# Performance work log

Measured on AMD Instinct MI355X. Metric: run time of the kernel, lower is better.

Reference implementation:

```python
import jax, jax.numpy as jnp
import numpy as np

B, C, H, W = 2, 256, 192, 192
STRIDE = 8


def conv2d(x, w, b, pad_h, pad_w):
    y = jax.lax.conv_general_dilated(
        x, w, window_strides=(1, 1),
        padding=[(pad_h, pad_h), (pad_w, pad_w)],
        dimension_numbers=('NCHW', 'OIHW', 'NCHW'))
    return y + b[None, :, None, None]


def rotated_feature_align(feat, boxes, spatial_scale):
    # feat: [B,C,Hf,Wf]; boxes: [B,Hf*Wf,5] per-pixel rboxes in image coords.
    # points=1: bilinearly sample feat at each pixel's box center and add to feat,
    # matching mmcv's rotated_feature_align forward kernel (incl. its (y,x) read order
    # and ROI-Align-style border handling).
    Bf, Cf, Hf, Wf = feat.shape
    y = boxes[..., 0].reshape(Bf, Hf, Wf) * spatial_scale
    x = boxes[..., 1].reshape(Bf, Hf, Wf) * spatial_scale
    valid = (y >= -1.0) & (y <= Hf) & (x >= -1.0) & (x <= Wf)
    y = jnp.maximum(y, 0.0)
    x = jnp.maximum(x, 0.0)
    yl0 = jnp.floor(y).astype(jnp.int32)
    xl0 = jnp.floor(x).astype(jnp.int32)
    ey = yl0 >= Hf - 1
    ex = xl0 >= Wf - 1
    yl = jnp.where(ey, Hf - 1, yl0)
    yh = jnp.where(ey, Hf - 1, jnp.minimum(yl0 + 1, Hf - 1))
    xl = jnp.where(ex, Wf - 1, xl0)
    xh = jnp.where(ex, Wf - 1, jnp.minimum(xl0 + 1, Wf - 1))
    y = jnp.where(ey, jnp.asarray(Hf - 1, feat.dtype), y)
    x = jnp.where(ex, jnp.asarray(Wf - 1, feat.dtype), x)
    ly = y - yl.astype(feat.dtype)
    lx = x - xl.astype(feat.dtype)
    hy = 1.0 - ly
    hx = 1.0 - lx
    ft = jnp.transpose(feat, (0, 2, 3, 1))  # [B,Hf,Wf,C]
    bi = jnp.arange(Bf)[:, None, None]
    v = ((hy * hx)[..., None] * ft[bi, yl, xl]
         + (hy * lx)[..., None] * ft[bi, yl, xh]
         + (ly * hx)[..., None] * ft[bi, yh, xl]
         + (ly * lx)[..., None] * ft[bi, yh, xh])
    v = jnp.where(valid[..., None], v, 0.0)
    return feat + jnp.transpose(v, (0, 3, 1, 2))


def setup_inputs() -> dict:
    key = jax.random.key(0)
    ks = jax.random.split(key, 9)
    x = jax.random.normal(ks[0], (B, C, H, W), dtype=jnp.float32)
    img = float(H * STRIDE)
    cy = jax.random.uniform(ks[1], (B, H * W), minval=0.0, maxval=img)
    cx = jax.random.uniform(ks[2], (B, H * W), minval=0.0, maxval=img)
    bw = jax.random.uniform(ks[3], (B, H * W), minval=8.0, maxval=64.0)
    bh = jax.random.uniform(ks[4], (B, H * W), minval=8.0, maxval=64.0)
    ba = jax.random.uniform(ks[5], (B, H * W), minval=-np.pi / 2, maxval=np.pi / 2)
    best_rbboxes = jnp.stack([cy, cx, bw, bh, ba], axis=-1)  # [B, H*W, 5]
    std = 0.01  # normal_init(std=0.01)
    w51 = jax.random.normal(ks[6], (C, C, 5, 1), dtype=jnp.float32) * std
    w15 = jax.random.normal(ks[7], (C, C, 1, 5), dtype=jnp.float32) * std
    w11 = jax.random.normal(ks[8], (C, C, 1, 1), dtype=jnp.float32) * std
    b51 = jnp.zeros((C,), jnp.float32)
    b15 = jnp.zeros((C,), jnp.float32)
    b11 = jnp.zeros((C,), jnp.float32)
    return {"x": x, "best_rbboxes": best_rbboxes, "w51": w51, "b51": b51,
            "w15": w15, "b15": b15, "w11": w11, "b11": b11}


def reference(x, best_rbboxes, w51, b51, w15, b15, w11, b11):
    # conv_5_1(conv_1_5(x)) + conv_1_1(x), then rotated feature alignment, then residual.
    feat = conv2d(conv2d(x, w15, b15, 0, 2), w51, b51, 2, 0) + conv2d(x, w11, b11, 0, 0)
    refined = rotated_feature_align(feat, best_rbboxes, 1.0 / STRIDE)
    return x + refined
```

## Files before the change

kernel.cpp:

```cpp
#include <hip/hip_runtime.h>
#include <hip/hip_bf16.h>
#include <stdint.h>

#define B_ 2
#define C_ 256
#define H_ 192
#define W_ 192
#define HW_ (H_*W_)
#define CHW_ (C_*HW_)
#define P_ (B_*HW_)
#define SCALE 0.125f

typedef __attribute__((ext_vector_type(8))) short bf16x8;
typedef __attribute__((ext_vector_type(4))) float f32x4;

__device__ __forceinline__ void gload_lds16(const void* g, void* l) {
  __builtin_amdgcn_global_load_lds(
      (const __attribute__((address_space(1))) uint32_t*)g,
      (__attribute__((address_space(3))) uint32_t*)l, 16, 0, 0);
}

__global__ __launch_bounds__(256) void wtrans_kernel(
    const float* __restrict__ w15, const float* __restrict__ w51,
    const float* __restrict__ w11,
    __hip_bfloat16* __restrict__ w1t, __hip_bfloat16* __restrict__ w2t,
    __hip_bfloat16* __restrict__ zbuf) {
  int i = blockIdx.x * 256 + threadIdx.x;
  if (i < C_ * C_ * 5) {
    int co = i / (C_ * 5);
    int r  = i - co * (C_ * 5);
    int ci = r / 5;
    int k  = r - ci * 5;
    w1t[(size_t)co * 1280 + k * 256 + ci] = __float2bfloat16(w15[i]);
    w2t[(size_t)co * 1536 + k * 256 + ci] = __float2bfloat16(w51[i]);
  }
  if (i < C_ * C_) {
    int co = i >> 8, ci = i & 255;
    w2t[(size_t)co * 1536 + 1280 + ci] = __float2bfloat16(w11[i]);
  }
  if (i < 1024) zbuf[i] = __float2bfloat16(0.f);
}

__global__ __launch_bounds__(256) void nchw2nhwc_kernel(
    const float* __restrict__ x, __hip_bfloat16* __restrict__ xT) {
  __shared__ float tile[64][65];
  const int p0 = blockIdx.x * 64, c0 = blockIdx.y * 64, b = blockIdx.z;
  const int tid = threadIdx.x;
  const float* xb = x + (size_t)b * CHW_;
  {
    const int cr = tid >> 4;
    const int pc = (tid & 15) * 4;
#pragma unroll
    for (int j = 0; j < 4; ++j) {
      float4 v = *(const float4*)(xb + (size_t)(c0 + cr + j * 16) * HW_ + p0 + pc);
      *(float4*)&tile[cr + j * 16][pc] = v;
    }
  }
  __syncthreads();
  {
    const int pr = tid >> 2;
    const int cc = (tid & 3) * 16;
    union { unsigned short u[16]; uint4 q[2]; } wpk;
#pragma unroll
    for (int j = 0; j < 16; ++j) {
      __hip_bfloat16 hb = __float2bfloat16(tile[cc + j][pr]);
      wpk.u[j] = *(unsigned short*)&hb;
    }
    char* xo = (char*)(xT + ((size_t)b * HW_ + p0 + pr) * C_ + c0 + cc);
    *(uint4*)xo = wpk.q[0];
    *(uint4*)(xo + 16) = wpk.q[1];
  }
}

#define AB1 25600
__global__ __launch_bounds__(256, 3) void gemm1_kernel(
    const __hip_bfloat16* __restrict__ xT, const __hip_bfloat16* __restrict__ w1t,
    const float* __restrict__ b15, __hip_bfloat16* __restrict__ t1,
    const __hip_bfloat16* __restrict__ zbuf) {
  __shared__ __align__(16) char lds[AB1 + 16384];
  int bid = blockIdx.x;
  bid = (bid & 7) * 96 + (bid >> 3);
  const int nb = bid & 1, bh = bid >> 1;
  const int p0 = bh * 192;
  const int tid = threadIdx.x, l = tid & 63, wid = tid >> 6;
  const int wrow = (wid >> 1) * 96, wcol = (wid & 1) * 64;
  const int sboff = (((l & 7) ^ (l >> 3)) << 4);
  const int lrow = l >> 3;
  const int corow0 = nb * 128;

  int b_ad[4][2];
#pragma unroll
  for (int n = 0; n < 4; ++n)
#pragma unroll
    for (int kk = 0; kk < 2; ++kk)
      b_ad[n][kk] = AB1 + (wcol + n * 16 + (l & 15)) * 128 +
                    (((kk * 4 + (l >> 4)) ^ ((l & 15) & 7)) << 4);

  f32x4 acc[6][4] = {};
  const char* xTb = (const char*)xT;
  const char* wB  = (const char*)w1t;
  const char* zb  = (const char*)zbuf;

  for (int cib = 0; cib < 4; ++cib) {
    for (int is = wid; is < 25; is += 4) {
      int row = is * 8 + lrow;
      const char* src = ((unsigned)(row - 4) < 192u)
          ? xTb + (size_t)(p0 + row - 4) * 512 + cib * 128 + sboff
          : zb + sboff;
      gload_lds16(src, lds + is * 1024);
    }
    for (int k = 0; k < 5; ++k) {
      int boff = k * 512 + cib * 128;
#pragma unroll
      for (int ii = 0; ii < 4; ++ii) {
        int is = wid * 4 + ii;
        const char* bs = wB + (size_t)(corow0 + is * 8 + lrow) * 2560 + boff + sboff;
        gload_lds16(bs, lds + AB1 + is * 1024);
      }
      __syncthreads();
      int x8 = ((l & 15) + k + 2) & 7;
      int arow0 = wrow + (l & 15) + k + 2;
#pragma unroll
      for (int kk = 0; kk < 2; ++kk) {
        int ablk = ((kk * 4 + (l >> 4)) ^ x8) << 4;
        bf16x8 bfr[4];
#pragma unroll
        for (int n = 0; n < 4; ++n) bfr[n] = *(const bf16x8*)(lds + b_ad[n][kk]);
#pragma unroll
        for (int m = 0; m < 6; ++m) {
          bf16x8 af = *(const bf16x8*)(lds + (arow0 + m * 16) * 128 + ablk);
#pragma unroll
          for (int n = 0; n < 4; ++n)
            acc[m][n] = __builtin_amdgcn_mfma_f32_16x16x32_bf16(af, bfr[n], acc[m][n], 0, 0, 0);
        }
      }
      __syncthreads();
    }
  }
#pragma unroll
  for (int n = 0; n < 4; ++n) {
    int co = corow0 + wcol + n * 16 + (l & 15);
    float bias = b15[co];
#pragma unroll
    for (int m = 0; m < 6; ++m) {
      int prow = p0 + wrow + m * 16 + (l >> 4) * 4;
#pragma unroll
      for (int r = 0; r < 4; ++r)
        t1[(size_t)(prow + r) * 256 + co] = __float2bfloat16(acc[m][n][r] + bias);
    }
  }
}

#define AB2 24576
__global__ __launch_bounds__(256, 3) void gemm2_kernel(
    const __hip_bfloat16* __restrict__ t1, const __hip_bfloat16* __restrict__ xT,
    const __hip_bfloat16* __restrict__ w2t,
    const float* __restrict__ b51, const float* __restrict__ b11,
    __hip_bfloat16* __restrict__ featT, const __hip_bfloat16* __restrict__ zbuf) {
  __shared__ __align__(16) char lds[AB2 + 16384];
  int bid = blockIdx.x;
  bid = (bid & 7) * 96 + (bid >> 3);
  const int nb = bid & 1, bh = bid >> 1;
  const int p0 = bh * 192;
  const int h = bh % 192;
  const int tid = threadIdx.x, l = tid & 63, wid = tid >> 6;
  const int wrow = (wid >> 1) * 96, wcol = (wid & 1) * 64;
  const int sboff = (((l & 7) ^ (l >> 3)) << 4);
  const int lrow = l >> 3;
  const int corow0 = nb * 128;

  int a_ad[6][2], b_ad[4][2];
#pragma unroll
  for (int m = 0; m < 6; ++m)
#pragma unroll
    for (int kk = 0; kk < 2; ++kk)
      a_ad[m][kk] = (wrow + m * 16 + (l & 15)) * 128 +
                    (((kk * 4 + (l >> 4)) ^ ((l & 15) & 7)) << 4);
#pragma unroll
  for (int n = 0; n < 4; ++n)
#pragma unroll
    for (int kk = 0; kk < 2; ++kk)
      b_ad[n][kk] = AB2 + (wcol + n * 16 + (l & 15)) * 128 +
                    (((kk * 4 + (l >> 4)) ^ ((l & 15) & 7)) << 4);

  f32x4 acc[6][4] = {};
  const char* t1b = (const char*)t1;
  const char* xTb = (const char*)xT;
  const char* wB  = (const char*)w2t;
  const char* zb  = (const char*)zbuf;

  for (int s = 0; s < 24; ++s) {
    const char* abase;
    int boff;
    if (s < 20) {
      int k = s >> 2, cib = s & 3, dl = k - 2;
      abase = ((unsigned)(h + dl) < 192u)
          ? t1b + (size_t)(p0 + dl * 192) * 512 + cib * 128
          : (const char*)0;
      boff = k * 512 + cib * 128;
    } else {
      abase = xTb + (size_t)p0 * 512 + (s - 20) * 128;
      boff = 2560 + (s - 20) * 128;
    }
    for (int is = wid; is < 24; is += 4) {
      int row = is * 8 + lrow;
      const char* src = abase ? abase + (size_t)row * 512 + sboff : zb + sboff;
      gload_lds16(src, lds + is * 1024);
    }
#pragma unroll
    for (int ii = 0; ii < 4; ++ii) {
      int is = wid * 4 + ii;
      const char* bs = wB + (size_t)(corow0 + is * 8 + lrow) * 3072 + boff + sboff;
      gload_lds16(bs, lds + AB2 + is * 1024);
    }
    __syncthreads();
#pragma unroll
    for (int kk = 0; kk < 2; ++kk) {
      bf16x8 bfr[4];
#pragma unroll
      for (int n = 0; n < 4; ++n) bfr[n] = *(const bf16x8*)(lds + b_ad[n][kk]);
#pragma unroll
      for (int m = 0; m < 6; ++m) {
        bf16x8 af = *(const bf16x8*)(lds + a_ad[m][kk]);
#pragma unroll
        for (int n = 0; n < 4; ++n)
          acc[m][n] = __builtin_amdgcn_mfma_f32_16x16x32_bf16(af, bfr[n], acc[m][n], 0, 0, 0);
      }
    }
    __syncthreads();
  }
#pragma unroll
  for (int n = 0; n < 4; ++n) {
    int co = corow0 + wcol + n * 16 + (l & 15);
    float bias = b51[co] + b11[co];
#pragma unroll
    for (int m = 0; m < 6; ++m) {
      int prow = p0 + wrow + m * 16 + (l >> 4) * 4;
#pragma unroll
      for (int r = 0; r < 4; ++r)
        featT[(size_t)(prow + r) * 256 + co] = __float2bfloat16(acc[m][n][r] + bias);
    }
  }
}

__global__ __launch_bounds__(256) void align_kernel(
    const __hip_bfloat16* __restrict__ xT, const __hip_bfloat16* __restrict__ featT,
    const float* __restrict__ boxes, float* __restrict__ out) {
  __shared__ float vs[16][258];
  const int tid = threadIdx.x, l = tid & 63, wv = tid >> 6;
  const int p0 = blockIdx.x * 16;

#pragma unroll
  for (int i = 0; i < 2; ++i) {
    int pl = wv * 4 + i * 2 + (l >> 5);
    int p = p0 + pl;
    int b = p / HW_;
    int p2 = p - b * HW_;
    float yy = boxes[(size_t)p * 5 + 0] * SCALE;
    float xx = boxes[(size_t)p * 5 + 1] * SCALE;
    bool valid = (yy >= -1.0f) && (yy <= (float)H_) && (xx >= -1.0f) && (xx <= (float)W_);
    yy = fmaxf(yy, 0.f);
    xx = fmaxf(xx, 0.f);
    int yl = (int)floorf(yy), xl = (int)floorf(xx);
    int yh, xh;
    if (yl >= H_ - 1) { yl = H_ - 1; yh = H_ - 1; yy = (float)(H_ - 1); } else { yh = yl + 1; }
    if (xl >= W_ - 1) { xl = W_ - 1; xh = W_ - 1; xx = (float)(W_ - 1); } else { xh = xl + 1; }
    float ly = yy - (float)yl, lx = xx - (float)xl;
    float hy = 1.f - ly, hx = 1.f - lx;
    float q00 = hy * hx, q01 = hy * lx, q10 = ly * hx, q11 = ly * lx;
    if (!valid) { q00 = 0.f; q01 = 0.f; q10 = 0.f; q11 = 0.f; }
    const unsigned short* fT = (const unsigned short*)featT + (size_t)b * HW_ * C_;
    const unsigned short* xb = (const unsigned short*)xT + (size_t)b * HW_ * C_;
    int co = (l & 31) * 8;
    uint4 A  = *(const uint4*)(fT + ((size_t)yl * W_ + xl) * C_ + co);
    uint4 Bv = *(const uint4*)(fT + ((size_t)yl * W_ + xh) * C_ + co);
    uint4 Cv = *(const uint4*)(fT + ((size_t)yh * W_ + xl) * C_ + co);
    uint4 D  = *(const uint4*)(fT + ((size_t)yh * W_ + xh) * C_ + co);
    uint4 E  = *(const uint4*)(fT + (size_t)p2 * C_ + co);
    uint4 X  = *(const uint4*)(xb + (size_t)p2 * C_ + co);
    float o[8];
#pragma unroll
    for (int w = 0; w < 4; ++w) {
      unsigned int aw = (&A.x)[w], bw = (&Bv.x)[w], cw = (&Cv.x)[w],
                   dw = (&D.x)[w], ew = (&E.x)[w], xw = (&X.x)[w];
      float a0 = __uint_as_float(aw << 16), a1 = __uint_as_float(aw & 0xffff0000u);
      float b0 = __uint_as_float(bw << 16), b1 = __uint_as_float(bw & 0xffff0000u);
      float c0 = __uint_as_float(cw << 16), c1 = __uint_as_float(cw & 0xffff0000u);
      float d0 = __uint_as_float(dw << 16), d1 = __uint_as_float(dw & 0xffff0000u);
      float e0 = __uint_as_float(ew << 16), e1 = __uint_as_float(ew & 0xffff0000u);
      float x0 = __uint_as_float(xw << 16), x1 = __uint_as_float(xw & 0xffff0000u);
      o[w * 2 + 0] = x0 + e0 + q00 * a0 + q01 * b0 + q10 * c0 + q11 * d0;
      o[w * 2 + 1] = x1 + e1 + q00 * a1 + q01 * b1 + q10 * c1 + q11 * d1;
    }
    *(float4*)&vs[pl][co]     = make_float4(o[0], o[1], o[2], o[3]);
    *(float4*)&vs[pl][co + 4] = make_float4(o[4], o[5], o[6], o[7]);
  }
  __syncthreads();

  const int pl = tid & 15, cg = tid >> 4;
  const int p = p0 + pl;
  const int b = p / HW_;
  const int p2 = p - b * HW_;
  float* oc = out + (size_t)b * CHW_ + p2;
#pragma unroll
  for (int j = 0; j < 16; ++j) {
    int ch = cg * 16 + j;
    __builtin_nontemporal_store(vs[pl][ch], &oc[(size_t)ch * HW_]);
  }
}

extern "C" void kernel_launch(void* const* d_in, const int* in_sizes, int n_in,
                              void* d_out, int out_size, void* d_ws, size_t ws_size,
                              hipStream_t stream) {
  const float* x     = (const float*)d_in[0];
  const float* boxes = (const float*)d_in[1];
  const float* w51   = (const float*)d_in[2];
  const float* b51   = (const float*)d_in[3];
  const float* w15   = (const float*)d_in[4];
  const float* b15   = (const float*)d_in[5];
  const float* w11   = (const float*)d_in[6];
  const float* b11   = (const float*)d_in[7];
  float* out = (float*)d_out;

  __hip_bfloat16* featT = (__hip_bfloat16*)d_ws;
  __hip_bfloat16* xT   = featT + (size_t)P_ * C_;
  __hip_bfloat16* w1t  = xT + (size_t)P_ * C_;
  __hip_bfloat16* w2t  = w1t + (size_t)C_ * 1280;
  __hip_bfloat16* zbuf = w2t + (size_t)C_ * 1536;
  __hip_bfloat16* t1 = (__hip_bfloat16*)d_out;

  wtrans_kernel<<<dim3((C_ * C_ * 5 + 255) / 256), 256, 0, stream>>>(
      w15, w51, w11, w1t, w2t, zbuf);
  nchw2nhwc_kernel<<<dim3(HW_ / 64, C_ / 64, B_), 256, 0, stream>>>(x, xT);
  gemm1_kernel<<<dim3(768), 256, 0, stream>>>(xT, w1t, b15, t1, zbuf);
  gemm2_kernel<<<dim3(768), 256, 0, stream>>>(t1, xT, w2t, b51, b11, featT, zbuf);
  align_kernel<<<dim3(P_ / 16), 256, 0, stream>>>(xT, featT, boxes, out);
}
```

Before: 172.5 us.

## Double-buffer gemm2 with 512-thread 384-row tiles and interleaved prefetch

Rewrites the second conv GEMM so each 512-thread block computes a 384-row by 128-channel tile, covering two image rows, with double-buffered LDS for A and B. The next K-step's global-to-LDS loads are issued in chunks between MFMA phases, replacing the old load-sync-compute-sync loop. Wave priority is raised around MFMA bursts and explicit waitcnts and barriers order the stages. The aim is to hide global load latency behind MFMA work. In exchange, the 128KB LDS allocation allows only one block per CU, and 384 blocks give an uneven final wave.

New measurement: 191.7 us. 11.1% more time.

```diff
diff --git a/kernel.cpp b/kernel.cpp
--- a/kernel.cpp
+++ b/kernel.cpp
@@ -151,83 +151,145 @@
   }
 }
 
-#define AB2 24576
-__global__ __launch_bounds__(256, 3) void gemm2_kernel(
+#define G2_AB 49152
+#define G2_BB 98304
+__global__ __launch_bounds__(512, 2) void gemm2_kernel(
     const __hip_bfloat16* __restrict__ t1, const __hip_bfloat16* __restrict__ xT,
     const __hip_bfloat16* __restrict__ w2t,
     const float* __restrict__ b51, const float* __restrict__ b11,
     __hip_bfloat16* __restrict__ featT, const __hip_bfloat16* __restrict__ zbuf) {
-  __shared__ __align__(16) char lds[AB2 + 16384];
+  __shared__ __align__(16) char lds[131072];
   int bid = blockIdx.x;
-  bid = (bid & 7) * 96 + (bid >> 3);
+  bid = (bid & 7) * 48 + (bid >> 3);
   const int nb = bid & 1, bh = bid >> 1;
-  const int p0 = bh * 192;
-  const int h = bh % 192;
+  const int p0 = bh * 384;
+  const int hv0 = (2 * bh) % 192;
   const int tid = threadIdx.x, l = tid & 63, wid = tid >> 6;
   const int wrow = (wid >> 1) * 96, wcol = (wid & 1) * 64;
   const int sboff = (((l & 7) ^ (l >> 3)) << 4);
   const int lrow = l >> 3;
   const int corow0 = nb * 128;
 
-  int a_ad[6][2], b_ad[4][2];
-#pragma unroll
-  for (int m = 0; m < 6; ++m)
-#pragma unroll
-    for (int kk = 0; kk < 2; ++kk)
-      a_ad[m][kk] = (wrow + m * 16 + (l & 15)) * 128 +
-                    (((kk * 4 + (l >> 4)) ^ ((l & 15) & 7)) << 4);
-#pragma unroll
-  for (int n = 0; n < 4; ++n)
-#pragma unroll
-    for (int kk = 0; kk < 2; ++kk)
-      b_ad[n][kk] = AB2 + (wcol + n * 16 + (l & 15)) * 128 +
-                    (((kk * 4 + (l >> 4)) ^ ((l & 15) & 7)) << 4);
-
-  f32x4 acc[6][4] = {};
   const char* t1b = (const char*)t1;
   const char* xTb = (const char*)xT;
   const char* wB  = (const char*)w2t;
   const char* zb  = (const char*)zbuf;
 
-  for (int s = 0; s < 24; ++s) {
-    const char* abase;
-    int boff;
+  auto stA = [&](int s, int buf, int i0, int i1) {
+    const char* base;
+    bool v0, v1;
     if (s < 20) {
       int k = s >> 2, cib = s & 3, dl = k - 2;
-      abase = ((unsigned)(h + dl) < 192u)
-          ? t1b + (size_t)(p0 + dl * 192) * 512 + cib * 128
-          : (const char*)0;
-      boff = k * 512 + cib * 128;
+      base = t1b + (ptrdiff_t)(p0 + dl * 192) * 512 + cib * 128;
+      v0 = (unsigned)(hv0 + dl) < 192u;
+      v1 = (unsigned)(hv0 + 1 + dl) < 192u;
     } else {
-      abase = xTb + (size_t)p0 * 512 + (s - 20) * 128;
-      boff = 2560 + (s - 20) * 128;
-    }
-    for (int is = wid; is < 24; is += 4) {
-      int row = is * 8 + lrow;
-      const char* src = abase ? abase + (size_t)row * 512 + sboff : zb + sboff;
-      gload_lds16(src, lds + is * 1024);
-    }
-#pragma unroll
-    for (int ii = 0; ii < 4; ++ii) {
-      int is = wid * 4 + ii;
-      const char* bs = wB + (size_t)(corow0 + is * 8 + lrow) * 3072 + boff + sboff;
-      gload_lds16(bs, lds + AB2 + is * 1024);
-    }
-    __syncthreads();
-#pragma unroll
-    for (int kk = 0; kk < 2; ++kk) {
-      bf16x8 bfr[4];
-#pragma unroll
-      for (int n = 0; n < 4; ++n) bfr[n] = *(const bf16x8*)(lds + b_ad[n][kk]);
-#pragma unroll
-      for (int m = 0; m < 6; ++m) {
-        bf16x8 af = *(const bf16x8*)(lds + a_ad[m][kk]);
-#pragma unroll
-        for (int n = 0; n < 4; ++n)
-          acc[m][n] = __builtin_amdgcn_mfma_f32_16x16x32_bf16(af, bfr[n], acc[m][n], 0, 0, 0);
-      }
-    }
-    __syncthreads();
+      base = xTb + (size_t)p0 * 512 + (s - 20) * 128;
+      v0 = v1 = true;
+    }
+#pragma unroll
+    for (int i = i0; i < i1; ++i) {
+      int slot = i * 8 + wid;
+      int row = slot * 8 + lrow;
+      bool ok = (row < 192) ? v0 : v1;
+      const char* src = ok ? base + (size_t)row * 512 + sboff : zb + sboff;
+      gload_lds16(src, lds + buf * G2_AB + slot * 1024);
+    }
+  };
+  auto stB = [&](int s, int buf) {
+    int boff = (s < 20) ? (s >> 2) * 512 + (s & 3) * 128 : 2560 + (s - 20) * 128;
+#pragma unroll
+    for (int i = 0; i < 2; ++i) {
+      int slot = i * 8 + wid;
+      const char* bs = wB + (size_t)(corow0 + slot * 8 + lrow) * 3072 + boff + sboff;
+      gload_lds16(bs, lds + G2_BB + buf * 16384 + slot * 1024);
+    }
+  };
+
+  int a_ad[6][2], b_ad[4][2];
+#pragma unroll
+  for (int m = 0; m < 6; ++m)
+#pragma unroll
+    for (int kk = 0; kk < 2; ++kk)
+      a_ad[m][kk] = (wrow + m * 16 + (l & 15)) * 128 +
+                    (((kk * 4 + (l >> 4)) ^ ((l & 15) & 7)) << 4);
+#pragma unroll
+  for (int n = 0; n < 4; ++n)
+#pragma unroll
+    for (int kk = 0; kk < 2; ++kk)
+      b_ad[n][kk] = (wcol + n * 16 + (l & 15)) * 128 +
+                    (((kk * 4 + (l >> 4)) ^ ((l & 15) & 7)) << 4);
+
+  f32x4 acc[6][4] = {};
+  stA(0, 0, 0, 6);
+  stB(0, 0);
+  asm volatile("s_waitcnt vmcnt(0)" ::: "memory");
+  __builtin_amdgcn_s_barrier();
+
+  for (int t = 0; t < 24; ++t) {
+    const int cur = t & 1, nxt = cur ^ 1;
+    const char* la = lds + cur * G2_AB;
+    const char* lb = lds + G2_BB + cur * 16384;
+    if (t > 0) asm volatile("s_waitcnt vmcnt(0)" ::: "memory");
+    bf16x8 af[6], bfr[2];
+#pragma unroll
+    for (int m = 0; m < 6; ++m) af[m] = *(const bf16x8*)(la + a_ad[m][0]);
+    bfr[0] = *(const bf16x8*)(lb + b_ad[0][0]);
+    bfr[1] = *(const bf16x8*)(lb + b_ad[1][0]);
+    if (t < 23) stA(t + 1, nxt, 0, 4);
+    __builtin_amdgcn_s_barrier();
+    asm volatile("s_waitcnt lgkmcnt(0)" ::: "memory");
+    __builtin_amdgcn_sched_barrier(0);
+    __builtin_amdgcn_s_setprio(1);
+#pragma unroll
+    for (int m = 0; m < 6; ++m) {
+      acc[m][0] = __builtin_amdgcn_mfma_f32_16x16x32_bf16(af[m], bfr[0], acc[m][0], 0, 0, 0);
+      acc[m][1] = __builtin_amdgcn_mfma_f32_16x16x32_bf16(af[m], bfr[1], acc[m][1], 0, 0, 0);
+    }
+    __builtin_amdgcn_s_setprio(0);
+    __builtin_amdgcn_s_barrier();
+    bfr[0] = *(const bf16x8*)(lb + b_ad[2][0]);
+    bfr[1] = *(const bf16x8*)(lb + b_ad[3][0]);
+    if (t < 23) { stA(t + 1, nxt, 4, 6); stB(t + 1, nxt); }
+    __builtin_amdgcn_s_barrier();
+    asm volatile("s_waitcnt lgkmcnt(0)" ::: "memory");
+    __builtin_amdgcn_sched_barrier(0);
+    __builtin_amdgcn_s_setprio(1);
+#pragma unroll
+    for (int m = 0; m < 6; ++m) {
+      acc[m][2] = __builtin_amdgcn_mfma_f32_16x16x32_bf16(af[m], bfr[0], acc[m][2], 0, 0, 0);
+      acc[m][3] = __builtin_amdgcn_mfma_f32_16x16x32_bf16(af[m], bfr[1], acc[m][3], 0, 0, 0);
+    }
+    __builtin_amdgcn_s_setprio(0);
+    __builtin_amdgcn_s_barrier();
+#pragma unroll
+    for (int m = 0; m < 6; ++m) af[m] = *(const bf16x8*)(la + a_ad[m][1]);
+    bfr[0] = *(const bf16x8*)(lb + b_ad[0][1]);
+    bfr[1] = *(const bf16x8*)(lb + b_ad[1][1]);
+    __builtin_amdgcn_s_barrier();
+    asm volatile("s_waitcnt lgkmcnt(0)" ::: "memory");
+    __builtin_amdgcn_sched_barrier(0);
+    __builtin_amdgcn_s_setprio(1);
+#pragma unroll
+    for (int m = 0; m < 6; ++m) {
+      acc[m][0] = __builtin_amdgcn_mfma_f32_16x16x32_bf16(af[m], bfr[0], acc[m][0], 0, 0, 0);
+      acc[m][1] = __builtin_amdgcn_mfma_f32_16x16x32_bf16(af[m], bfr[1], acc[m][1], 0, 0, 0);
+    }
+    __builtin_amdgcn_s_setprio(0);
+    __builtin_amdgcn_s_barrier();
+    bfr[0] = *(const bf16x8*)(lb + b_ad[2][1]);
+    bfr[1] = *(const bf16x8*)(lb + b_ad[3][1]);
+    __builtin_amdgcn_s_barrier();
+    asm volatile("s_waitcnt lgkmcnt(0)" ::: "memory");
+    __builtin_amdgcn_sched_barrier(0);
+    __builtin_amdgcn_s_setprio(1);
+#pragma unroll
+    for (int m = 0; m < 6; ++m) {
+      acc[m][2] = __builtin_amdgcn_mfma_f32_16x16x32_bf16(af[m], bfr[0], acc[m][2], 0, 0, 0);
+      acc[m][3] = __builtin_amdgcn_mfma_f32_16x16x32_bf16(af[m], bfr[1], acc[m][3], 0, 0, 0);
+    }
+    __builtin_amdgcn_s_setprio(0);
+    __builtin_amdgcn_s_barrier();
   }
 #pragma unroll
   for (int n = 0; n < 4; ++n) {
@@ -333,6 +395,6 @@
       w15, w51, w11, w1t, w2t, zbuf);
   nchw2nhwc_kernel<<<dim3(HW_ / 64, C_ / 64, B_), 256, 0, stream>>>(x, xT);
   gemm1_kernel<<<dim3(768), 256, 0, stream>>>(xT, w1t, b15, t1, zbuf);
-  gemm2_kernel<<<dim3(768), 256, 0, stream>>>(t1, xT, w2t, b51, b11, featT, zbuf);
+  gemm2_kernel<<<dim3(384), 512, 0, stream>>>(t1, xT, w2t, b51, b11, featT, zbuf);
   align_kernel<<<dim3(P_ / 16), 256, 0, stream>>>(xT, featT, boxes, out);
 }
```
